# Kernel optimization log

Measured on AMD Instinct MI355X. Metric: run time of the kernel, lower is better.

## Reference

```python
import jax, jax.numpy as jnp
import numpy as np

B, S, U = 64, 64, 16
EMB = 10
D = U - 2 + 2 * EMB      # encoder d_model = 34
DD = 3                   # decoder d_model
FF = 4                   # dim_feedforward
NL = 4                   # num layers (enc and dec)
ENH = 2                  # encoder heads
WV, SV = 10000, 400      # word / syllable vocab sizes


def _ln(x, w, b, eps=1e-5):
    mu = jnp.mean(x, -1, keepdims=True)
    var = jnp.mean((x - mu) ** 2, -1, keepdims=True)
    return (x - mu) / jnp.sqrt(var + eps) * w + b


def _mha(xq, xkv, qkv_w, qkv_b, out_w, out_b, nhead, mask=None):
    d = xq.shape[-1]
    wq, wk, wv = jnp.split(qkv_w, 3, axis=0)
    bq, bk, bv = jnp.split(qkv_b, 3, axis=0)
    q = xq @ wq.T + bq
    k = xkv @ wk.T + bk
    v = xkv @ wv.T + bv
    b_, sq, sk = q.shape[0], q.shape[1], k.shape[1]
    dh = d // nhead
    q = q.reshape(b_, sq, nhead, dh)
    k = k.reshape(b_, sk, nhead, dh)
    v = v.reshape(b_, sk, nhead, dh)
    scores = jnp.einsum('bqhd,bkhd->bhqk', q, k) * (1.0 / np.sqrt(dh))
    if mask is not None:
        scores = scores + mask
    attn = jax.nn.softmax(scores, axis=-1)
    out = jnp.einsum('bhqk,bkhd->bqhd', attn, v).reshape(b_, sq, d)
    return out @ out_w.T + out_b


def _pos_encoding(batch, d_model):
    # Faithful to the original quirk: pe has shape [max_len, 1, d] and is added
    # to a batch-first [B,S,D] tensor as x + pe[:B]  ->  row b of pe is added
    # to ALL sequence positions of batch element b.
    pos = jnp.arange(batch, dtype=jnp.float32)[:, None]
    div = jnp.exp(jnp.arange(0, d_model, 2, dtype=jnp.float32) * (-np.log(10000.0) / d_model))
    ang = pos * div  # [B, D/2]
    pe = jnp.stack([jnp.sin(ang), jnp.cos(ang)], axis=-1).reshape(batch, d_model)
    return pe[:, None, :]  # [B,1,D]


def setup_inputs() -> dict:
    key = jax.random.key(0)
    ks = iter(jax.random.split(key, 64))

    def n(shape, s=0.1):
        return jax.random.normal(next(ks), shape, dtype=jnp.float32) * s

    base = jax.random.uniform(next(ks), (B, S, U), dtype=jnp.float32)
    widx = jax.random.randint(next(ks), (B, S), 0, WV).astype(jnp.float32)
    sidx = jax.random.randint(next(ks), (B, S), 0, SV).astype(jnp.float32)
    src = base.at[:, :, U - 2].set(widx).at[:, :, U - 1].set(sidx)
    return {
        'src': src,
        'word_emb': jax.random.uniform(next(ks), (WV, EMB), jnp.float32, -0.1, 0.1),
        'syll_emb': jax.random.uniform(next(ks), (SV, EMB), jnp.float32, -0.1, 0.1),
        'enc_qkv_w': n((NL, 3 * D, D)), 'enc_qkv_b': jnp.zeros((NL, 3 * D)),
        'enc_out_w': n((NL, D, D)), 'enc_out_b': jnp.zeros((NL, D)),
        'enc_ln1_w': jnp.ones((NL, D)), 'enc_ln1_b': jnp.zeros((NL, D)),
        'enc_lin1_w': n((NL, FF, D)), 'enc_lin1_b': jnp.zeros((NL, FF)),
        'enc_lin2_w': n((NL, D, FF)), 'enc_lin2_b': jnp.zeros((NL, D)),
        'enc_ln2_w': jnp.ones((NL, D)), 'enc_ln2_b': jnp.zeros((NL, D)),
        'norm_w': jnp.ones((D,)), 'norm_b': jnp.zeros((D,)),
        'eo_w': jax.random.uniform(next(ks), (DD, D), jnp.float32, -0.1, 0.1),
        'eo_b': jnp.zeros((DD,)),
        'dec_sa_qkv_w': n((NL, 3 * DD, DD)), 'dec_sa_qkv_b': jnp.zeros((NL, 3 * DD)),
        'dec_sa_out_w': n((NL, DD, DD)), 'dec_sa_out_b': jnp.zeros((NL, DD)),
        'dec_ln1_w': jnp.ones((NL, DD)), 'dec_ln1_b': jnp.zeros((NL, DD)),
        'dec_ca_qkv_w': n((NL, 3 * DD, DD)), 'dec_ca_qkv_b': jnp.zeros((NL, 3 * DD)),
        'dec_ca_out_w': n((NL, DD, DD)), 'dec_ca_out_b': jnp.zeros((NL, DD)),
        'dec_ln2_w': jnp.ones((NL, DD)), 'dec_ln2_b': jnp.zeros((NL, DD)),
        'dec_lin1_w': n((NL, FF, DD)), 'dec_lin1_b': jnp.zeros((NL, FF)),
        'dec_lin2_w': n((NL, DD, FF)), 'dec_lin2_b': jnp.zeros((NL, DD)),
        'dec_ln3_w': jnp.ones((NL, DD)), 'dec_ln3_b': jnp.zeros((NL, DD)),
    }


def reference(src, word_emb, syll_emb,
              enc_qkv_w, enc_qkv_b, enc_out_w, enc_out_b,
              enc_ln1_w, enc_ln1_b, enc_lin1_w, enc_lin1_b,
              enc_lin2_w, enc_lin2_b, enc_ln2_w, enc_ln2_b,
              norm_w, norm_b, eo_w, eo_b,
              dec_sa_qkv_w, dec_sa_qkv_b, dec_sa_out_w, dec_sa_out_b,
              dec_ln1_w, dec_ln1_b,
              dec_ca_qkv_w, dec_ca_qkv_b, dec_ca_out_w, dec_ca_out_b,
              dec_ln2_w, dec_ln2_b,
              dec_lin1_w, dec_lin1_b, dec_lin2_w, dec_lin2_b,
              dec_ln3_w, dec_ln3_b):
    b, s = src.shape[0], src.shape[1]
    # embed_lyrics
    widx = src[:, :, U - 2].astype(jnp.int32)
    sidx = src[:, :, U - 1].astype(jnp.int32)
    x = jnp.concatenate([src[:, :, :U - 2], word_emb[widx], syll_emb[sidx]], axis=2)  # [B,S,D]
    x = x + _pos_encoding(b, D)
    # TransformerEncoder (post-norm, relu, dropout=0) + final LayerNorm
    for l in range(NL):
        sa = _mha(x, x, enc_qkv_w[l], enc_qkv_b[l], enc_out_w[l], enc_out_b[l], ENH)
        x = _ln(x + sa, enc_ln1_w[l], enc_ln1_b[l])
        ff = jax.nn.relu(x @ enc_lin1_w[l].T + enc_lin1_b[l]) @ enc_lin2_w[l].T + enc_lin2_b[l]
        x = _ln(x + ff, enc_ln2_w[l], enc_ln2_b[l])
    x = _ln(x, norm_w, norm_b)
    memory = x @ eo_w.T + eo_b  # [B,S,3]

    causal = jnp.where(jnp.tril(jnp.ones((s, s), bool)), 0.0, -1e9).astype(jnp.float32)

    def decode(tgt):
        y = tgt
        for l in range(NL):
            sa = _mha(y, y, dec_sa_qkv_w[l], dec_sa_qkv_b[l], dec_sa_out_w[l], dec_sa_out_b[l], 1, causal)
            y = _ln(y + sa, dec_ln1_w[l], dec_ln1_b[l])
            ca = _mha(y, memory, dec_ca_qkv_w[l], dec_ca_qkv_b[l], dec_ca_out_w[l], dec_ca_out_b[l], 1)
            y = _ln(y + ca, dec_ln2_w[l], dec_ln2_b[l])
            ff = jax.nn.relu(y @ dec_lin1_w[l].T + dec_lin1_b[l]) @ dec_lin2_w[l].T + dec_lin2_b[l]
            y = _ln(y + ff, dec_ln3_w[l], dec_ln3_b[l])
        return y

    # mask, position i only depends on tgt[:, :i+1], so a fixed-size padded
    # buffer + scan computes identical values.
    def step(tgt, i):
        out_i = jax.lax.dynamic_slice_in_dim(decode(tgt), i, 1, axis=1)  # [B,1,3]
        return jax.lax.dynamic_update_slice(tgt, out_i, (0, i + 1, 0)), None

    tgt0 = jnp.zeros((b, s, DD), jnp.float32)
    tgt, _ = jax.lax.scan(step, tgt0, jnp.arange(s - 1))
    return jnp.concatenate([tgt, src[:, :, U - 2:U - 1], src[:, :, U - 1:U]], axis=2)
```

## Files before the change

kernel.cpp:

```cpp
#include <hip/hip_runtime.h>
#include <math.h>

#define B_ 64
#define S_ 64
#define U_ 16
#define EMB_ 10
#define D_ 34
#define DD_ 3
#define FF_ 4
#define NL_ 4

typedef float v2f __attribute__((ext_vector_type(2)));

__global__ __launch_bounds__(512) void enc_kernel(
    const float* __restrict__ src, const float* __restrict__ wemb,
    const float* __restrict__ semb,
    const float* __restrict__ qkv_w, const float* __restrict__ qkv_b,
    const float* __restrict__ out_w, const float* __restrict__ out_b,
    const float* __restrict__ ln1_w, const float* __restrict__ ln1_b,
    const float* __restrict__ lin1_w, const float* __restrict__ lin1_b,
    const float* __restrict__ lin2_w, const float* __restrict__ lin2_b,
    const float* __restrict__ ln2_w, const float* __restrict__ ln2_b,
    const float* __restrict__ norm_w, const float* __restrict__ norm_b,
    const float* __restrict__ eo_w, const float* __restrict__ eo_b,
    float* __restrict__ mem, float* __restrict__ out)
{
    const int b = blockIdx.x;
    const int tid = threadIdx.x;
    const int wv_ = tid >> 6;
    const int lane = tid & 63;

    __shared__ float xs[S_][D_ + 1];
    __shared__ float tmp[S_][D_ + 1];
    __shared__ float att[S_][D_ + 1];
    __shared__ __align__(16) float qsh[2][S_][21];
    __shared__ __align__(16) float ksh[2][S_][20];
    __shared__ __align__(16) float vsh[2][S_][20];
    __shared__ float ffh[S_][5];
    __shared__ float pacc[4][128][19];

    const float rs17 = 0.24253562503633297f;
    const float negln = -logf(10000.0f) / (float)D_;

    #pragma unroll
    for (int rr = 0; rr < 5; ++rr) {
        int idx = tid + rr * 512;
        if (idx < S_ * D_) {
            int pos = idx / D_, d = idx % D_;
            float v;
            if (d < U_ - 2) {
                v = src[(b * S_ + pos) * U_ + d];
            } else if (d < U_ - 2 + EMB_) {
                int wi = (int)src[(b * S_ + pos) * U_ + (U_ - 2)];
                v = wemb[wi * EMB_ + (d - (U_ - 2))];
            } else {
                int si = (int)src[(b * S_ + pos) * U_ + (U_ - 1)];
                v = semb[si * EMB_ + (d - (U_ - 2 + EMB_))];
            }
            int k = d >> 1;
            float div = __expf((float)(2 * k) * negln);
            float ang = (float)b * div;
            v += (d & 1) ? __cosf(ang) : __sinf(ang);
            xs[pos][d] = v;
        }
    }
    __syncthreads();

    for (int l = 0; l < NL_; ++l) {
        const float* Wq = qkv_w + l * 3 * D_ * D_;
        const float* Bq = qkv_b + l * 3 * D_;

        {
            v2f xr2[17];
            #pragma unroll
            for (int d2 = 0; d2 < 17; ++d2) {
                v2f t; t.x = xs[lane][2 * d2]; t.y = xs[lane][2 * d2 + 1];
                xr2[d2] = t;
            }
            #pragma unroll
            for (int rb = 0; rb < 13; ++rb) {
                int r = wv_ + (rb << 3);
                if (r < 3 * D_) {
                    int ru = __builtin_amdgcn_readfirstlane(r);
                    const v2f* w2 = (const v2f*)(Wq + ru * D_);
                    v2f a2; a2.x = Bq[ru]; a2.y = 0.f;
                    #pragma unroll
                    for (int d2 = 0; d2 < 17; ++d2)
                        a2 = __builtin_elementwise_fma(xr2[d2], w2[d2], a2);
                    float acc = a2.x + a2.y;
                    if (ru < D_)          { int h = (ru >= 17), dd = ru - h * 17; qsh[h][lane][dd] = acc; }
                    else if (ru < 2 * D_) { int rr2 = ru - D_;     int h = (rr2 >= 17), dd = rr2 - h * 17; ksh[h][lane][dd] = acc; }
                    else                  { int rr2 = ru - 2 * D_; int h = (rr2 >= 17), dd = rr2 - h * 17; vsh[h][lane][dd] = acc; }
                }
            }
        }
        __syncthreads();

        {
            int c = tid >> 7, hq = tid & 127;
            int h = hq >> 6, qi = hq & 63;
            float qv[17], acc[17];
            #pragma unroll
            for (int d = 0; d < 17; ++d) { qv[d] = qsh[h][qi][d]; acc[d] = 0.f; }
            float ssum = 0.f;
            int j0 = c * 16;
            #pragma unroll 4
            for (int jj = 0; jj < 16; ++jj) {
                int j = j0 + jj;
                const float4* kr = (const float4*)ksh[h][j];
                const float4* vr = (const float4*)vsh[h][j];
                float4 k0 = kr[0], k1 = kr[1], k2 = kr[2], k3 = kr[3];
                float  k16 = ksh[h][j][16];
                float4 v0 = vr[0], v1 = vr[1], v2 = vr[2], v3 = vr[3];
                float  v16 = vsh[h][j][16];
                float sE = qv[0]*k0.x + qv[2]*k0.z + qv[4]*k1.x + qv[6]*k1.z +
                           qv[8]*k2.x + qv[10]*k2.z + qv[12]*k3.x + qv[14]*k3.z;
                float sO = qv[1]*k0.y + qv[3]*k0.w + qv[5]*k1.y + qv[7]*k1.w +
                           qv[9]*k2.y + qv[11]*k2.w + qv[13]*k3.y + qv[15]*k3.w;
                float sc = sE + sO + qv[16]*k16;
                float e = __expf(sc * rs17);
                ssum += e;
                acc[0] += e*v0.x;  acc[1] += e*v0.y;  acc[2] += e*v0.z;  acc[3] += e*v0.w;
                acc[4] += e*v1.x;  acc[5] += e*v1.y;  acc[6] += e*v1.z;  acc[7] += e*v1.w;
                acc[8] += e*v2.x;  acc[9] += e*v2.y;  acc[10] += e*v2.z; acc[11] += e*v2.w;
                acc[12] += e*v3.x; acc[13] += e*v3.y; acc[14] += e*v3.z; acc[15] += e*v3.w;
                acc[16] += e*v16;
            }
            #pragma unroll
            for (int d = 0; d < 17; ++d) pacc[c][hq][d] = acc[d];
            pacc[c][hq][17] = ssum;
        }
        __syncthreads();

        if (tid < 128) {
            int h = tid >> 6, qi = tid & 63;
            int off = h * 17;
            float ssum = pacc[0][tid][17] + pacc[1][tid][17] +
                         pacc[2][tid][17] + pacc[3][tid][17];
            float inv = 1.f / ssum;
            #pragma unroll
            for (int d = 0; d < 17; ++d)
                att[qi][off + d] = (pacc[0][tid][d] + pacc[1][tid][d] +
                                    pacc[2][tid][d] + pacc[3][tid][d]) * inv;
        }
        __syncthreads();

        {
            v2f ar2[17];
            #pragma unroll
            for (int d2 = 0; d2 < 17; ++d2) {
                v2f t; t.x = att[lane][2 * d2]; t.y = att[lane][2 * d2 + 1];
                ar2[d2] = t;
            }
            const float* Wo = out_w + l * D_ * D_;
            const float* Bo = out_b + l * D_;
            #pragma unroll
            for (int rb = 0; rb < 5; ++rb) {
                int d = wv_ + (rb << 3);
                if (d < D_) {
                    int du = __builtin_amdgcn_readfirstlane(d);
                    const v2f* w2 = (const v2f*)(Wo + du * D_);
                    v2f a2; a2.x = Bo[du]; a2.y = 0.f;
                    #pragma unroll
                    for (int d2 = 0; d2 < 17; ++d2)
                        a2 = __builtin_elementwise_fma(ar2[d2], w2[d2], a2);
                    tmp[lane][du] = xs[lane][du] + a2.x + a2.y;
                }
            }
        }
        __syncthreads();

        {
            int row = tid >> 3, sub = tid & 7;
            float s = 0.f, sq = 0.f;
            #pragma unroll
            for (int d = sub; d < D_; d += 8) { float t = tmp[row][d]; s += t; sq = fmaf(t, t, sq); }
            #pragma unroll
            for (int m = 1; m < 8; m <<= 1) { s += __shfl_xor(s, m, 8); sq += __shfl_xor(sq, m, 8); }
            float mu = s * (1.0f / D_);
            float var = fmaf(sq, 1.0f / D_, -mu * mu);
            float rstd = rsqrtf(var + 1e-5f);
            #pragma unroll
            for (int d = sub; d < D_; d += 8)
                xs[row][d] = (tmp[row][d] - mu) * rstd * ln1_w[l * D_ + d] + ln1_b[l * D_ + d];
        }
        __syncthreads();

        if (wv_ < 4) {
            int fu = __builtin_amdgcn_readfirstlane(wv_);
            const v2f* w2 = (const v2f*)(lin1_w + l * FF_ * D_ + fu * D_);
            v2f a2; a2.x = lin1_b[l * FF_ + fu]; a2.y = 0.f;
            #pragma unroll
            for (int d2 = 0; d2 < 17; ++d2) {
                v2f t; t.x = xs[lane][2 * d2]; t.y = xs[lane][2 * d2 + 1];
                a2 = __builtin_elementwise_fma(t, w2[d2], a2);
            }
            ffh[lane][fu] = fmaxf(a2.x + a2.y, 0.f);
        }
        __syncthreads();

        {
            float h0 = ffh[lane][0], h1 = ffh[lane][1],
                  h2 = ffh[lane][2], h3 = ffh[lane][3];
            const float* W2 = lin2_w + l * D_ * FF_;
            const float* B2 = lin2_b + l * D_;
            #pragma unroll
            for (int rb = 0; rb < 5; ++rb) {
                int d = wv_ + (rb << 3);
                if (d < D_) {
                    int du = __builtin_amdgcn_readfirstlane(d);
                    const float* wrow = W2 + du * FF_;
                    float acc = fmaf(h0, wrow[0], fmaf(h1, wrow[1],
                                fmaf(h2, wrow[2], fmaf(h3, wrow[3], B2[du]))));
                    tmp[lane][du] = xs[lane][du] + acc;
                }
            }
        }
        __syncthreads();

        {
            int row = tid >> 3, sub = tid & 7;
            float s = 0.f, sq = 0.f;
            #pragma unroll
            for (int d = sub; d < D_; d += 8) { float t = tmp[row][d]; s += t; sq = fmaf(t, t, sq); }
            #pragma unroll
            for (int m = 1; m < 8; m <<= 1) { s += __shfl_xor(s, m, 8); sq += __shfl_xor(sq, m, 8); }
            float mu = s * (1.0f / D_);
            float var = fmaf(sq, 1.0f / D_, -mu * mu);
            float rstd = rsqrtf(var + 1e-5f);
            #pragma unroll
            for (int d = sub; d < D_; d += 8)
                xs[row][d] = (tmp[row][d] - mu) * rstd * ln2_w[l * D_ + d] + ln2_b[l * D_ + d];
        }
        __syncthreads();
    }

    {
        int row = tid >> 3, sub = tid & 7;
        float s = 0.f, sq = 0.f;
        #pragma unroll
        for (int d = sub; d < D_; d += 8) { float t = xs[row][d]; s += t; sq = fmaf(t, t, sq); }
        #pragma unroll
        for (int m = 1; m < 8; m <<= 1) { s += __shfl_xor(s, m, 8); sq += __shfl_xor(sq, m, 8); }
        float mu = s * (1.0f / D_);
        float var = fmaf(sq, 1.0f / D_, -mu * mu);
        float rstd = rsqrtf(var + 1e-5f);
        #pragma unroll
        for (int d = sub; d < D_; d += 8)
            tmp[row][d] = (xs[row][d] - mu) * rstd * norm_w[d] + norm_b[d];
    }
    __syncthreads();

    if (wv_ < 3) {
        int ru = __builtin_amdgcn_readfirstlane(wv_);
        const v2f* w2 = (const v2f*)(eo_w + ru * D_);
        v2f a2; a2.x = eo_b[ru]; a2.y = 0.f;
        #pragma unroll
        for (int d2 = 0; d2 < 17; ++d2) {
            v2f t; t.x = tmp[lane][2 * d2]; t.y = tmp[lane][2 * d2 + 1];
            a2 = __builtin_elementwise_fma(t, w2[d2], a2);
        }
        mem[(b * S_ + lane) * DD_ + ru] = a2.x + a2.y;
    }

    if (tid < S_) {
        out[(b * S_ + tid) * 5 + 3] = src[(b * S_ + tid) * U_ + (U_ - 2)];
        out[(b * S_ + tid) * 5 + 4] = src[(b * S_ + tid) * U_ + (U_ - 1)];
    }
}

#define PIN(x) asm volatile("" : "+v"(x))

template <int CTRL>
__device__ __forceinline__ float dpp_add(float v) {
    int t = __builtin_amdgcn_update_dpp(0, __float_as_int(v), CTRL, 0xf, 0xf, true);
    return v + __int_as_float(t);
}

__device__ __forceinline__ float red16(float v) {
    v = dpp_add<0x111>(v);
    v = dpp_add<0x112>(v);
    v = dpp_add<0x114>(v);
    v = dpp_add<0x118>(v);
    return v;
}

__device__ __forceinline__ float rlane(float v, int l) {
    return __int_as_float(__builtin_amdgcn_readlane(__float_as_int(v), l));
}

__device__ __forceinline__ void ln3e(float z0, float z1, float z2,
                                     float w0, float w1, float w2,
                                     float b0, float b1, float b2,
                                     float& o0, float& o1, float& o2) {
    float s1 = (z0 + z1) + z2;
    float s2 = fmaf(z0, z0, fmaf(z1, z1, z2 * z2));
    float mu = s1 * (1.0f / 3.0f);
    float vpe = fmaf(s2, (1.0f / 3.0f), fmaf(-mu, mu, 1e-5f));
    float rstd = __builtin_amdgcn_rsqf(vpe);
    o0 = fmaf(z0 - mu, rstd * w0, b0);
    o1 = fmaf(z1 - mu, rstd * w1, b1);
    o2 = fmaf(z2 - mu, rstd * w2, b2);
}

__global__ __launch_bounds__(64, 1) void dec_kernel(
    const float* __restrict__ mem,
    const float* __restrict__ sa_qkv_w, const float* __restrict__ sa_qkv_b,
    const float* __restrict__ sa_out_w, const float* __restrict__ sa_out_b,
    const float* __restrict__ gln1_w, const float* __restrict__ gln1_b,
    const float* __restrict__ ca_qkv_w, const float* __restrict__ ca_qkv_b,
    const float* __restrict__ ca_out_w, const float* __restrict__ ca_out_b,
    const float* __restrict__ gln2_w, const float* __restrict__ gln2_b,
    const float* __restrict__ l1_w, const float* __restrict__ l1_b,
    const float* __restrict__ l2_w, const float* __restrict__ l2_b,
    const float* __restrict__ gln3_w, const float* __restrict__ gln3_b,
    float* __restrict__ out)
{
    const int b = blockIdx.x;
    const int lane = threadIdx.x;
    const float LOG2E = 1.4426950408889634f;
    const float rs3 = 0.5773502691896258f;
    const float QS = rs3 * LOG2E;

    __shared__ __align__(16) float fst[NL_][40];
    for (int t = lane; t < NL_ * 40; t += 64) {
        int l = t / 40, s = t % 40;
        float v = 0.f;
        if      (s < 12) v = l1_w[l * 12 + s];
        else if (s < 16) v = l1_b[l * 4 + (s - 12)];
        else if (s < 28) v = l2_w[l * 12 + (s - 16)];
        else if (s < 31) v = l2_b[l * 3 + (s - 28)];
        else if (s < 34) v = gln3_w[l * 3 + (s - 31)];
        else if (s < 37) v = gln3_b[l * 3 + (s - 34)];
        fst[l][s] = v;
    }
    __syncthreads();

    float Wsq[NL_][9][3], Bsq[NL_][9];
    float Wso[NL_][3][3], Bso[NL_][3];
    float N1w[NL_][3], N1b[NL_][3];
    float N2w[NL_][3], N2b[NL_][3];
    float Bco[NL_][3];
    float cu[NL_][3];
    float cb[NL_];
    float cvp[NL_][3];

    #pragma unroll
    for (int l = 0; l < NL_; ++l) {
        #pragma unroll
        for (int r = 0; r < 9; ++r) {
            float sc = (r < 3) ? QS : 1.0f;
            Bsq[l][r] = sa_qkv_b[l * 9 + r] * sc;
            #pragma unroll
            for (int c = 0; c < 3; ++c) Wsq[l][r][c] = sa_qkv_w[l * 27 + r * 3 + c] * sc;
        }
        #pragma unroll
        for (int r = 0; r < 3; ++r) {
            Bso[l][r] = sa_out_b[l * 3 + r];
            Bco[l][r] = ca_out_b[l * 3 + r];
            N1w[l][r] = gln1_w[l * 3 + r];  N1b[l][r] = gln1_b[l * 3 + r];
            N2w[l][r] = gln2_w[l * 3 + r];  N2b[l][r] = gln2_b[l * 3 + r];
            #pragma unroll
            for (int c = 0; c < 3; ++c) Wso[l][r][c] = sa_out_w[l * 9 + r * 3 + c];
        }
    }

    float m0 = mem[(b * S_ + lane) * DD_ + 0];
    float m1 = mem[(b * S_ + lane) * DD_ + 1];
    float m2 = mem[(b * S_ + lane) * DD_ + 2];

    #pragma unroll
    for (int l = 0; l < NL_; ++l) {
        float ck[3], cv[3];
        #pragma unroll
        for (int r = 0; r < 3; ++r) {
            ck[r] = ca_qkv_w[l * 27 + (3 + r) * 3 + 0] * m0 +
                    ca_qkv_w[l * 27 + (3 + r) * 3 + 1] * m1 +
                    ca_qkv_w[l * 27 + (3 + r) * 3 + 2] * m2 + ca_qkv_b[l * 9 + 3 + r];
            cv[r] = ca_qkv_w[l * 27 + (6 + r) * 3 + 0] * m0 +
                    ca_qkv_w[l * 27 + (6 + r) * 3 + 1] * m1 +
                    ca_qkv_w[l * 27 + (6 + r) * 3 + 2] * m2 + ca_qkv_b[l * 9 + 6 + r];
        }
        #pragma unroll
        for (int s = 0; s < 3; ++s)
            cu[l][s] = QS * (ca_qkv_w[l * 27 + 0 + s] * ck[0] +
                             ca_qkv_w[l * 27 + 3 + s] * ck[1] +
                             ca_qkv_w[l * 27 + 6 + s] * ck[2]);
        cb[l] = QS * (ca_qkv_b[l * 9 + 0] * ck[0] +
                      ca_qkv_b[l * 9 + 1] * ck[1] +
                      ca_qkv_b[l * 9 + 2] * ck[2]);
        #pragma unroll
        for (int r = 0; r < 3; ++r)
            cvp[l][r] = ca_out_w[l * 9 + r * 3 + 0] * cv[0] +
                        ca_out_w[l * 9 + r * 3 + 1] * cv[1] +
                        ca_out_w[l * 9 + r * 3 + 2] * cv[2];
    }

    #pragma unroll
    for (int l = 0; l < NL_; ++l) {
        #pragma unroll
        for (int r = 0; r < 9; ++r) {
            PIN(Bsq[l][r]);
            #pragma unroll
            for (int c = 0; c < 3; ++c) PIN(Wsq[l][r][c]);
        }
        PIN(cb[l]);
        #pragma unroll
        for (int r = 0; r < 3; ++r) {
            PIN(Bso[l][r]); PIN(Bco[l][r]);
            PIN(N1w[l][r]); PIN(N1b[l][r]); PIN(N2w[l][r]); PIN(N2b[l][r]);
            PIN(cu[l][r]);  PIN(cvp[l][r]);
            #pragma unroll
            for (int c = 0; c < 3; ++c) PIN(Wso[l][r][c]);
        }
    }

    float sk[NL_][3] = {{0.f}}, sv[NL_][3] = {{0.f}};

    if (lane < 3) out[(b * S_ + 0) * 5 + lane] = 0.f;

    float y0 = 0.f, y1 = 0.f, y2 = 0.f;

    for (int i = 0; i < S_ - 1; ++i) {
        float msa = (lane <= i) ? 0.f : -1.0e30f;
        #pragma unroll
        for (int l = 0; l < NL_; ++l) {
            float wv[40];
            {
                const float4* fp = (const float4*)fst[l];
                #pragma unroll
                for (int k = 0; k < 10; ++k) {
                    float4 t4 = fp[k];
                    wv[4 * k + 0] = t4.x; wv[4 * k + 1] = t4.y;
                    wv[4 * k + 2] = t4.z; wv[4 * k + 3] = t4.w;
                }
            }

            float q[3], kn[3], vn[3], vp[3];
            #pragma unroll
            for (int r = 0; r < 3; ++r) {
                kn[r] = fmaf(Wsq[l][3 + r][0], y0, fmaf(Wsq[l][3 + r][1], y1, fmaf(Wsq[l][3 + r][2], y2, Bsq[l][3 + r])));
                q[r]  = fmaf(Wsq[l][r][0], y0, fmaf(Wsq[l][r][1], y1, fmaf(Wsq[l][r][2], y2, Bsq[l][r])));
                vn[r] = fmaf(Wsq[l][6 + r][0], y0, fmaf(Wsq[l][6 + r][1], y1, fmaf(Wsq[l][6 + r][2], y2, Bsq[l][6 + r])));
            }
            #pragma unroll
            for (int r = 0; r < 3; ++r)
                vp[r] = fmaf(Wso[l][r][0], vn[0], fmaf(Wso[l][r][1], vn[1], Wso[l][r][2] * vn[2]));
            if (lane == i) {
                #pragma unroll
                for (int r = 0; r < 3; ++r) { sk[l][r] = kn[r]; sv[l][r] = vp[r]; }
            }
            float sc = fmaf(q[0], sk[l][0], fmaf(q[1], sk[l][1], fmaf(q[2], sk[l][2], msa)));
            float e = __builtin_amdgcn_exp2f(sc);
            float se  = red16(e);
            float sa0 = red16(e * sv[l][0]);
            float sa1 = red16(e * sv[l][1]);
            float sa2 = red16(e * sv[l][2]);
            int rl = 15;
            if (i >= 15) {
                se  = dpp_add<0x142>(se);  sa0 = dpp_add<0x142>(sa0);
                sa1 = dpp_add<0x142>(sa1); sa2 = dpp_add<0x142>(sa2);
                rl = 31;
            }
            if (i >= 31) {
                se  = dpp_add<0x143>(se);  sa0 = dpp_add<0x143>(sa0);
                sa1 = dpp_add<0x143>(sa1); sa2 = dpp_add<0x143>(sa2);
                rl = 63;
            }
            float yb0 = y0 + Bso[l][0], yb1 = y1 + Bso[l][1], yb2 = y2 + Bso[l][2];
            float es = rlane(se, rl);
            float S0 = rlane(sa0, rl), S1 = rlane(sa1, rl), S2 = rlane(sa2, rl);
            float inv = __builtin_amdgcn_rcpf(es);
            ln3e(fmaf(S0, inv, yb0), fmaf(S1, inv, yb1), fmaf(S2, inv, yb2),
                 N1w[l][0], N1w[l][1], N1w[l][2], N1b[l][0], N1b[l][1], N1b[l][2],
                 y0, y1, y2);

            float sc2 = fmaf(y0, cu[l][0], fmaf(y1, cu[l][1], fmaf(y2, cu[l][2], cb[l])));
            float e2 = __builtin_amdgcn_exp2f(sc2);
            float ce  = red16(e2);
            float ca0 = red16(e2 * cvp[l][0]);
            float ca1 = red16(e2 * cvp[l][1]);
            float ca2 = red16(e2 * cvp[l][2]);
            ce  = dpp_add<0x142>(ce);  ca0 = dpp_add<0x142>(ca0);
            ca1 = dpp_add<0x142>(ca1); ca2 = dpp_add<0x142>(ca2);
            ce  = dpp_add<0x143>(ce);  ca0 = dpp_add<0x143>(ca0);
            ca1 = dpp_add<0x143>(ca1); ca2 = dpp_add<0x143>(ca2);
            float yc0 = y0 + Bco[l][0], yc1 = y1 + Bco[l][1], yc2 = y2 + Bco[l][2];
            float cs = rlane(ce, 63);
            float C0 = rlane(ca0, 63), C1 = rlane(ca1, 63), C2 = rlane(ca2, 63);
            float inv2 = __builtin_amdgcn_rcpf(cs);
            ln3e(fmaf(C0, inv2, yc0), fmaf(C1, inv2, yc1), fmaf(C2, inv2, yc2),
                 N2w[l][0], N2w[l][1], N2w[l][2], N2b[l][0], N2b[l][1], N2b[l][2],
                 y0, y1, y2);

            #pragma unroll
            for (int k = 0; k < 37; ++k) PIN(wv[k]);
            float h0 = fmaxf(fmaf(wv[0], y0, fmaf(wv[1],  y1, fmaf(wv[2],  y2, wv[12]))), 0.f);
            float h1 = fmaxf(fmaf(wv[3], y0, fmaf(wv[4],  y1, fmaf(wv[5],  y2, wv[13]))), 0.f);
            float h2 = fmaxf(fmaf(wv[6], y0, fmaf(wv[7],  y1, fmaf(wv[8],  y2, wv[14]))), 0.f);
            float h3 = fmaxf(fmaf(wv[9], y0, fmaf(wv[10], y1, fmaf(wv[11], y2, wv[15]))), 0.f);
            float yf0 = y0 + wv[28], yf1 = y1 + wv[29], yf2 = y2 + wv[30];
            float f0 = fmaf(wv[16], h0, fmaf(wv[17], h1, fmaf(wv[18], h2, fmaf(wv[19], h3, yf0))));
            float f1 = fmaf(wv[20], h0, fmaf(wv[21], h1, fmaf(wv[22], h2, fmaf(wv[23], h3, yf1))));
            float f2 = fmaf(wv[24], h0, fmaf(wv[25], h1, fmaf(wv[26], h2, fmaf(wv[27], h3, yf2))));
            ln3e(f0, f1, f2,
                 wv[31], wv[32], wv[33], wv[34], wv[35], wv[36],
                 y0, y1, y2);
        }
        if (lane == 0) {
            out[(b * S_ + i + 1) * 5 + 0] = y0;
            out[(b * S_ + i + 1) * 5 + 1] = y1;
            out[(b * S_ + i + 1) * 5 + 2] = y2;
        }
    }
}

extern "C" void kernel_launch(void* const* d_in, const int* in_sizes, int n_in,
                              void* d_out, int out_size, void* d_ws, size_t ws_size,
                              hipStream_t stream) {
    const float* src  = (const float*)d_in[0];
    const float* wemb = (const float*)d_in[1];
    const float* semb = (const float*)d_in[2];

    float* mem = (float*)d_ws;
    float* out = (float*)d_out;

    enc_kernel<<<B_, 512, 0, stream>>>(
        src, wemb, semb,
        (const float*)d_in[3],  (const float*)d_in[4],
        (const float*)d_in[5],  (const float*)d_in[6],
        (const float*)d_in[7],  (const float*)d_in[8],
        (const float*)d_in[9],  (const float*)d_in[10],
        (const float*)d_in[11], (const float*)d_in[12],
        (const float*)d_in[13], (const float*)d_in[14],
        (const float*)d_in[15], (const float*)d_in[16],
        (const float*)d_in[17], (const float*)d_in[18],
        mem, out);

    dec_kernel<<<B_, 64, 0, stream>>>(
        mem,
        (const float*)d_in[19], (const float*)d_in[20],
        (const float*)d_in[21], (const float*)d_in[22],
        (const float*)d_in[23], (const float*)d_in[24],
        (const float*)d_in[25], (const float*)d_in[26],
        (const float*)d_in[27], (const float*)d_in[28],
        (const float*)d_in[29], (const float*)d_in[30],
        (const float*)d_in[31], (const float*)d_in[32],
        (const float*)d_in[33], (const float*)d_in[34],
        (const float*)d_in[35], (const float*)d_in[36],
        out);
}
```

Before: 327.3 us.

## Fold layernorm affine into cross-attn and FFN weights; split decode loop by reduction width

The LN1 affine parameters are folded into the cross-attention query projection, and the LN2 affine into the first FFN layer. The cross-attention score and the FFN hidden units are then computed from centered values scaled by rstd, which shortens the serial dependency chain at each decode step. The step loop is split into three template-specialized ranges so the self-attention reduction width and readlane index are compile-time constants instead of runtime branches. The cost is larger code size and slightly different floating-point rounding.

Measured after the change: 316.2 us. 1.04x faster.

```diff
diff --git a/kernel.cpp b/kernel.cpp
--- a/kernel.cpp
+++ b/kernel.cpp
@@ -271,6 +271,8 @@
 
 #define PIN(x) asm volatile("" : "+v"(x))
 
+template <int N> struct IC { static constexpr int value = N; };
+
 template <int CTRL>
 __device__ __forceinline__ float dpp_add(float v) {
     int t = __builtin_amdgcn_update_dpp(0, __float_as_int(v), CTRL, 0xf, 0xf, true);
@@ -285,8 +287,9 @@
     return v;
 }
 
-__device__ __forceinline__ float rlane(float v, int l) {
-    return __int_as_float(__builtin_amdgcn_readlane(__float_as_int(v), l));
+template <int L>
+__device__ __forceinline__ float rlane(float v) {
+    return __int_as_float(__builtin_amdgcn_readlane(__float_as_int(v), L));
 }
 
 __device__ __forceinline__ void ln3e(float z0, float z1, float z2,
@@ -326,8 +329,13 @@
     for (int t = lane; t < NL_ * 40; t += 64) {
         int l = t / 40, s = t % 40;
         float v = 0.f;
-        if      (s < 12) v = l1_w[l * 12 + s];
-        else if (s < 16) v = l1_b[l * 4 + (s - 12)];
+        if      (s < 12) v = l1_w[l * 12 + s] * gln2_w[l * 3 + (s % 3)];
+        else if (s < 16) {
+            int j = s - 12;
+            v = l1_w[l * 12 + j * 3 + 0] * gln2_b[l * 3 + 0] +
+                l1_w[l * 12 + j * 3 + 1] * gln2_b[l * 3 + 1] +
+                l1_w[l * 12 + j * 3 + 2] * gln2_b[l * 3 + 2] + l1_b[l * 4 + j];
+        }
         else if (s < 28) v = l2_w[l * 12 + (s - 16)];
         else if (s < 31) v = l2_b[l * 3 + (s - 28)];
         else if (s < 34) v = gln3_w[l * 3 + (s - 31)];
@@ -341,8 +349,9 @@
     float N1w[NL_][3], N1b[NL_][3];
     float N2w[NL_][3], N2b[NL_][3];
     float Bco[NL_][3];
-    float cu[NL_][3];
-    float cb[NL_];
+    float wcu[NL_][3];
+    float swcu[NL_];
+    float cbb[NL_];
     float cvp[NL_][3];
 
     #pragma unroll
@@ -371,7 +380,7 @@
 
     #pragma unroll
     for (int l = 0; l < NL_; ++l) {
-        float ck[3], cv[3];
+        float ck[3], cv[3], cuv[3];
         #pragma unroll
         for (int r = 0; r < 3; ++r) {
             ck[r] = ca_qkv_w[l * 27 + (3 + r) * 3 + 0] * m0 +
@@ -383,17 +392,21 @@
         }
         #pragma unroll
         for (int s = 0; s < 3; ++s)
-            cu[l][s] = QS * (ca_qkv_w[l * 27 + 0 + s] * ck[0] +
-                             ca_qkv_w[l * 27 + 3 + s] * ck[1] +
-                             ca_qkv_w[l * 27 + 6 + s] * ck[2]);
-        cb[l] = QS * (ca_qkv_b[l * 9 + 0] * ck[0] +
-                      ca_qkv_b[l * 9 + 1] * ck[1] +
-                      ca_qkv_b[l * 9 + 2] * ck[2]);
+            cuv[s] = QS * (ca_qkv_w[l * 27 + 0 + s] * ck[0] +
+                           ca_qkv_w[l * 27 + 3 + s] * ck[1] +
+                           ca_qkv_w[l * 27 + 6 + s] * ck[2]);
+        float cbv = QS * (ca_qkv_b[l * 9 + 0] * ck[0] +
+                          ca_qkv_b[l * 9 + 1] * ck[1] +
+                          ca_qkv_b[l * 9 + 2] * ck[2]);
         #pragma unroll
         for (int r = 0; r < 3; ++r)
             cvp[l][r] = ca_out_w[l * 9 + r * 3 + 0] * cv[0] +
                         ca_out_w[l * 9 + r * 3 + 1] * cv[1] +
                         ca_out_w[l * 9 + r * 3 + 2] * cv[2];
+        #pragma unroll
+        for (int r = 0; r < 3; ++r) wcu[l][r] = cuv[r] * N1w[l][r];
+        swcu[l] = wcu[l][0] + wcu[l][1] + wcu[l][2];
+        cbb[l]  = cbv + cuv[0] * N1b[l][0] + cuv[1] * N1b[l][1] + cuv[2] * N1b[l][2];
     }
 
     #pragma unroll
@@ -404,12 +417,12 @@
             #pragma unroll
             for (int c = 0; c < 3; ++c) PIN(Wsq[l][r][c]);
         }
-        PIN(cb[l]);
+        PIN(swcu[l]); PIN(cbb[l]);
         #pragma unroll
         for (int r = 0; r < 3; ++r) {
             PIN(Bso[l][r]); PIN(Bco[l][r]);
             PIN(N1w[l][r]); PIN(N1b[l][r]); PIN(N2w[l][r]); PIN(N2b[l][r]);
-            PIN(cu[l][r]);  PIN(cvp[l][r]);
+            PIN(wcu[l][r]); PIN(cvp[l][r]);
             #pragma unroll
             for (int c = 0; c < 3; ++c) PIN(Wso[l][r][c]);
         }
@@ -421,98 +434,123 @@
 
     float y0 = 0.f, y1 = 0.f, y2 = 0.f;
 
-    for (int i = 0; i < S_ - 1; ++i) {
-        float msa = (lane <= i) ? 0.f : -1.0e30f;
-        #pragma unroll
-        for (int l = 0; l < NL_; ++l) {
-            float wv[40];
-            {
-                const float4* fp = (const float4*)fst[l];
+    auto run_range = [&](int ibeg, int iend, auto nstc) {
+        constexpr int NST = decltype(nstc)::value;
+        constexpr int RL = (NST == 4) ? 15 : (NST == 5) ? 31 : 63;
+        for (int i = ibeg; i < iend; ++i) {
+            float msa = (lane <= i) ? 0.f : -1.0e30f;
+            bool isme = (lane == i);
+            #pragma unroll
+            for (int l = 0; l < NL_; ++l) {
+                float wv[40];
+                {
+                    const float4* fp = (const float4*)fst[l];
+                    #pragma unroll
+                    for (int k = 0; k < 10; ++k) {
+                        float4 t4 = fp[k];
+                        wv[4 * k + 0] = t4.x; wv[4 * k + 1] = t4.y;
+                        wv[4 * k + 2] = t4.z; wv[4 * k + 3] = t4.w;
+                    }
+                }
+
+                float q[3], kn[3], vn[3], vp[3];
                 #pragma unroll
-                for (int k = 0; k < 10; ++k) {
-                    float4 t4 = fp[k];
-                    wv[4 * k + 0] = t4.x; wv[4 * k + 1] = t4.y;
-                    wv[4 * k + 2] = t4.z; wv[4 * k + 3] = t4.w;
-                }
-            }
-
-            float q[3], kn[3], vn[3], vp[3];
-            #pragma unroll
-            for (int r = 0; r < 3; ++r) {
-                kn[r] = fmaf(Wsq[l][3 + r][0], y0, fmaf(Wsq[l][3 + r][1], y1, fmaf(Wsq[l][3 + r][2], y2, Bsq[l][3 + r])));
-                q[r]  = fmaf(Wsq[l][r][0], y0, fmaf(Wsq[l][r][1], y1, fmaf(Wsq[l][r][2], y2, Bsq[l][r])));
-                vn[r] = fmaf(Wsq[l][6 + r][0], y0, fmaf(Wsq[l][6 + r][1], y1, fmaf(Wsq[l][6 + r][2], y2, Bsq[l][6 + r])));
-            }
-            #pragma unroll
-            for (int r = 0; r < 3; ++r)
-                vp[r] = fmaf(Wso[l][r][0], vn[0], fmaf(Wso[l][r][1], vn[1], Wso[l][r][2] * vn[2]));
-            if (lane == i) {
+                for (int r = 0; r < 3; ++r) {
+                    kn[r] = fmaf(Wsq[l][3 + r][0], y0, fmaf(Wsq[l][3 + r][1], y1, fmaf(Wsq[l][3 + r][2], y2, Bsq[l][3 + r])));
+                    q[r]  = fmaf(Wsq[l][r][0], y0, fmaf(Wsq[l][r][1], y1, fmaf(Wsq[l][r][2], y2, Bsq[l][r])));
+                    vn[r] = fmaf(Wsq[l][6 + r][0], y0, fmaf(Wsq[l][6 + r][1], y1, fmaf(Wsq[l][6 + r][2], y2, Bsq[l][6 + r])));
+                }
                 #pragma unroll
-                for (int r = 0; r < 3; ++r) { sk[l][r] = kn[r]; sv[l][r] = vp[r]; }
-            }
-            float sc = fmaf(q[0], sk[l][0], fmaf(q[1], sk[l][1], fmaf(q[2], sk[l][2], msa)));
-            float e = __builtin_amdgcn_exp2f(sc);
-            float se  = red16(e);
-            float sa0 = red16(e * sv[l][0]);
-            float sa1 = red16(e * sv[l][1]);
-            float sa2 = red16(e * sv[l][2]);
-            int rl = 15;
-            if (i >= 15) {
-                se  = dpp_add<0x142>(se);  sa0 = dpp_add<0x142>(sa0);
-                sa1 = dpp_add<0x142>(sa1); sa2 = dpp_add<0x142>(sa2);
-                rl = 31;
-            }
-            if (i >= 31) {
-                se  = dpp_add<0x143>(se);  sa0 = dpp_add<0x143>(sa0);
-                sa1 = dpp_add<0x143>(sa1); sa2 = dpp_add<0x143>(sa2);
-                rl = 63;
-            }
-            float yb0 = y0 + Bso[l][0], yb1 = y1 + Bso[l][1], yb2 = y2 + Bso[l][2];
-            float es = rlane(se, rl);
-            float S0 = rlane(sa0, rl), S1 = rlane(sa1, rl), S2 = rlane(sa2, rl);
-            float inv = __builtin_amdgcn_rcpf(es);
-            ln3e(fmaf(S0, inv, yb0), fmaf(S1, inv, yb1), fmaf(S2, inv, yb2),
-                 N1w[l][0], N1w[l][1], N1w[l][2], N1b[l][0], N1b[l][1], N1b[l][2],
-                 y0, y1, y2);
-
-            float sc2 = fmaf(y0, cu[l][0], fmaf(y1, cu[l][1], fmaf(y2, cu[l][2], cb[l])));
-            float e2 = __builtin_amdgcn_exp2f(sc2);
-            float ce  = red16(e2);
-            float ca0 = red16(e2 * cvp[l][0]);
-            float ca1 = red16(e2 * cvp[l][1]);
-            float ca2 = red16(e2 * cvp[l][2]);
-            ce  = dpp_add<0x142>(ce);  ca0 = dpp_add<0x142>(ca0);
-            ca1 = dpp_add<0x142>(ca1); ca2 = dpp_add<0x142>(ca2);
-            ce  = dpp_add<0x143>(ce);  ca0 = dpp_add<0x143>(ca0);
-            ca1 = dpp_add<0x143>(ca1); ca2 = dpp_add<0x143>(ca2);
-            float yc0 = y0 + Bco[l][0], yc1 = y1 + Bco[l][1], yc2 = y2 + Bco[l][2];
-            float cs = rlane(ce, 63);
-            float C0 = rlane(ca0, 63), C1 = rlane(ca1, 63), C2 = rlane(ca2, 63);
-            float inv2 = __builtin_amdgcn_rcpf(cs);
-            ln3e(fmaf(C0, inv2, yc0), fmaf(C1, inv2, yc1), fmaf(C2, inv2, yc2),
-                 N2w[l][0], N2w[l][1], N2w[l][2], N2b[l][0], N2b[l][1], N2b[l][2],
-                 y0, y1, y2);
-
-            #pragma unroll
-            for (int k = 0; k < 37; ++k) PIN(wv[k]);
-            float h0 = fmaxf(fmaf(wv[0], y0, fmaf(wv[1],  y1, fmaf(wv[2],  y2, wv[12]))), 0.f);
-            float h1 = fmaxf(fmaf(wv[3], y0, fmaf(wv[4],  y1, fmaf(wv[5],  y2, wv[13]))), 0.f);
-            float h2 = fmaxf(fmaf(wv[6], y0, fmaf(wv[7],  y1, fmaf(wv[8],  y2, wv[14]))), 0.f);
-            float h3 = fmaxf(fmaf(wv[9], y0, fmaf(wv[10], y1, fmaf(wv[11], y2, wv[15]))), 0.f);
-            float yf0 = y0 + wv[28], yf1 = y1 + wv[29], yf2 = y2 + wv[30];
-            float f0 = fmaf(wv[16], h0, fmaf(wv[17], h1, fmaf(wv[18], h2, fmaf(wv[19], h3, yf0))));
-            float f1 = fmaf(wv[20], h0, fmaf(wv[21], h1, fmaf(wv[22], h2, fmaf(wv[23], h3, yf1))));
-            float f2 = fmaf(wv[24], h0, fmaf(wv[25], h1, fmaf(wv[26], h2, fmaf(wv[27], h3, yf2))));
-            ln3e(f0, f1, f2,
-                 wv[31], wv[32], wv[33], wv[34], wv[35], wv[36],
-                 y0, y1, y2);
-        }
-        if (lane == 0) {
-            out[(b * S_ + i + 1) * 5 + 0] = y0;
-            out[(b * S_ + i + 1) * 5 + 1] = y1;
-            out[(b * S_ + i + 1) * 5 + 2] = y2;
-        }
-    }
+                for (int r = 0; r < 3; ++r)
+                    vp[r] = fmaf(Wso[l][r][0], vn[0], fmaf(Wso[l][r][1], vn[1], Wso[l][r][2] * vn[2]));
+                if (isme) {
+                    #pragma unroll
+                    for (int r = 0; r < 3; ++r) { sk[l][r] = kn[r]; sv[l][r] = vp[r]; }
+                }
+                float sc = fmaf(q[0], sk[l][0], fmaf(q[1], sk[l][1], fmaf(q[2], sk[l][2], msa)));
+                float e = __builtin_amdgcn_exp2f(sc);
+                float se  = red16(e);
+                float sa0 = red16(e * sv[l][0]);
+                float sa1 = red16(e * sv[l][1]);
+                float sa2 = red16(e * sv[l][2]);
+                if constexpr (NST >= 5) {
+                    se  = dpp_add<0x142>(se);  sa0 = dpp_add<0x142>(sa0);
+                    sa1 = dpp_add<0x142>(sa1); sa2 = dpp_add<0x142>(sa2);
+                }
+                if constexpr (NST >= 6) {
+                    se  = dpp_add<0x143>(se);  sa0 = dpp_add<0x143>(sa0);
+                    sa1 = dpp_add<0x143>(sa1); sa2 = dpp_add<0x143>(sa2);
+                }
+                float yb0 = y0 + Bso[l][0], yb1 = y1 + Bso[l][1], yb2 = y2 + Bso[l][2];
+                float es = rlane<RL>(se);
+                float S0 = rlane<RL>(sa0), S1 = rlane<RL>(sa1), S2 = rlane<RL>(sa2);
+                float inv = __builtin_amdgcn_rcpf(es);
+                float z0 = fmaf(S0, inv, yb0), z1 = fmaf(S1, inv, yb1), z2v = fmaf(S2, inv, yb2);
+
+                float s1m = (z0 + z1) + z2v;
+                float mu = s1m * (1.0f / 3.0f);
+                float zw = fmaf(z0, wcu[l][0], fmaf(z1, wcu[l][1], z2v * wcu[l][2]));
+                float inner = fmaf(-mu, swcu[l], zw);
+                float s2m = fmaf(z0, z0, fmaf(z1, z1, z2v * z2v));
+                float vpe = fmaf(s2m, (1.0f / 3.0f), fmaf(-mu, mu, 1e-5f));
+                float rstd1 = __builtin_amdgcn_rsqf(vpe);
+                float sc2 = fmaf(rstd1, inner, cbb[l]);
+                float e2 = __builtin_amdgcn_exp2f(sc2);
+                float ce  = red16(e2);
+                float ca0 = red16(e2 * cvp[l][0]);
+                float ca1 = red16(e2 * cvp[l][1]);
+                float ca2 = red16(e2 * cvp[l][2]);
+                ce  = dpp_add<0x142>(ce);  ca0 = dpp_add<0x142>(ca0);
+                ca1 = dpp_add<0x142>(ca1); ca2 = dpp_add<0x142>(ca2);
+                ce  = dpp_add<0x143>(ce);  ca0 = dpp_add<0x143>(ca0);
+                ca1 = dpp_add<0x143>(ca1); ca2 = dpp_add<0x143>(ca2);
+                float y1_0 = fmaf(z0 - mu, rstd1 * N1w[l][0], N1b[l][0]);
+                float y1_1 = fmaf(z1 - mu, rstd1 * N1w[l][1], N1b[l][1]);
+                float y1_2 = fmaf(z2v - mu, rstd1 * N1w[l][2], N1b[l][2]);
+                float yc0 = y1_0 + Bco[l][0], yc1 = y1_1 + Bco[l][1], yc2 = y1_2 + Bco[l][2];
+                float cs = rlane<63>(ce);
+                float C0 = rlane<63>(ca0), C1 = rlane<63>(ca1), C2 = rlane<63>(ca2);
+                float inv2 = __builtin_amdgcn_rcpf(cs);
+                float g0 = fmaf(C0, inv2, yc0), g1 = fmaf(C1, inv2, yc1), g2 = fmaf(C2, inv2, yc2);
+
+                float t1m = (g0 + g1) + g2;
+                float mu2 = t1m * (1.0f / 3.0f);
+                float c20 = g0 - mu2, c21 = g1 - mu2, c22 = g2 - mu2;
+                float t2m = fmaf(g0, g0, fmaf(g1, g1, g2 * g2));
+                float vpe2 = fmaf(t2m, (1.0f / 3.0f), fmaf(-mu2, mu2, 1e-5f));
+                float rstd2 = __builtin_amdgcn_rsqf(vpe2);
+                #pragma unroll
+                for (int k = 0; k < 37; ++k) PIN(wv[k]);
+                float d0 = fmaf(wv[0], c20, fmaf(wv[1],  c21, wv[2]  * c22));
+                float d1 = fmaf(wv[3], c20, fmaf(wv[4],  c21, wv[5]  * c22));
+                float d2 = fmaf(wv[6], c20, fmaf(wv[7],  c21, wv[8]  * c22));
+                float d3 = fmaf(wv[9], c20, fmaf(wv[10], c21, wv[11] * c22));
+                float h0 = fmaxf(fmaf(rstd2, d0, wv[12]), 0.f);
+                float h1 = fmaxf(fmaf(rstd2, d1, wv[13]), 0.f);
+                float h2 = fmaxf(fmaf(rstd2, d2, wv[14]), 0.f);
+                float h3 = fmaxf(fmaf(rstd2, d3, wv[15]), 0.f);
+                float y2_0 = fmaf(c20, rstd2 * N2w[l][0], N2b[l][0]);
+                float y2_1 = fmaf(c21, rstd2 * N2w[l][1], N2b[l][1]);
+                float y2_2 = fmaf(c22, rstd2 * N2w[l][2], N2b[l][2]);
+                float yf0 = y2_0 + wv[28], yf1 = y2_1 + wv[29], yf2 = y2_2 + wv[30];
+                float f0 = fmaf(wv[16], h0, fmaf(wv[17], h1, fmaf(wv[18], h2, fmaf(wv[19], h3, yf0))));
+                float f1 = fmaf(wv[20], h0, fmaf(wv[21], h1, fmaf(wv[22], h2, fmaf(wv[23], h3, yf1))));
+                float f2 = fmaf(wv[24], h0, fmaf(wv[25], h1, fmaf(wv[26], h2, fmaf(wv[27], h3, yf2))));
+                ln3e(f0, f1, f2,
+                     wv[31], wv[32], wv[33], wv[34], wv[35], wv[36],
+                     y0, y1, y2);
+            }
+            if (lane == 0) {
+                out[(b * S_ + i + 1) * 5 + 0] = y0;
+                out[(b * S_ + i + 1) * 5 + 1] = y1;
+                out[(b * S_ + i + 1) * 5 + 2] = y2;
+            }
+        }
+    };
+
+    run_range(0, 15, IC<4>{});
+    run_range(15, 31, IC<5>{});
+    run_range(31, S_ - 1, IC<6>{});
 }
 
 extern "C" void kernel_launch(void* const* d_in, const int* in_sizes, int n_in,
```
